# Kernel optimization log

Measured on AMD Instinct MI355X. Metric: run time of the kernel, lower is better.

Reference implementation:

```python
import jax, jax.numpy as jnp
import numpy as np

NIN, NOUT = 256, 64

def setup_inputs() -> dict:
    key = jax.random.key(0)
    k1, k2, k3, k4 = jax.random.split(key, 4)
    B, T = 4, 4096
    y = jax.random.normal(k1, (B, T, NIN), dtype=jnp.float32)
    # torch Linear(nin, nout).weight has shape [nout, nin]; store as [nin, nout]
    s = 1.0 / np.sqrt(NIN)
    Wq = jax.random.uniform(k2, (NIN, NOUT), jnp.float32, -s, s)
    Wk = jax.random.uniform(k3, (NIN, NOUT), jnp.float32, -s, s)
    Wv = jax.random.uniform(k4, (NIN, NOUT), jnp.float32, -s, s)
    return {"y": y, "Wq": Wq, "Wk": Wk, "Wv": Wv}

def reference(y, Wq, Wk, Wv):
    T = y.shape[1]
    que = y @ Wq  # [B,T,NOUT]
    key = y @ Wk
    val = y @ Wv
    att = jnp.einsum('bqd,bkd->bqk', que, key)  # [B,T,T]
    causal = jnp.tril(jnp.ones((T, T), dtype=bool))  # True = keep
    att = jnp.where(causal, att, -jnp.inf)
    att = jax.nn.softmax(att / jnp.sqrt(jnp.float32(NOUT)), axis=-1)
    return jnp.einsum('bqk,bkd->bqd', att, val)
```

## Files before the change

### kernel.cpp

```cpp
#include <hip/hip_runtime.h>
#include <hip/hip_bf16.h>

#define TLEN 4096
#define NINP 256
#define DD   64

#define QSCALE 0.18033688011112042f

typedef __attribute__((ext_vector_type(8))) short bf16x8;
typedef __attribute__((ext_vector_type(4))) short bf16x4;
typedef __attribute__((ext_vector_type(4))) float f32x4;

union U8 { bf16x8 v; uint u[4]; };
union U4 { bf16x4 v; uint u[2]; };

__device__ inline ushort bfu(float x) {
    union { float f; uint u; } a; a.f = x;
    uint r = a.u + 0x7fffu + ((a.u >> 16) & 1u);
    return (ushort)(r >> 16);
}
__device__ inline uint pk2(float lo, float hi) {
    return (uint)bfu(lo) | ((uint)bfu(hi) << 16);
}

__device__ inline bf16x8 ld16(const ushort* p) {
    return *(const bf16x8*)p;
}
__device__ inline bf16x8 ld8x2(const ushort* p) {
    U8 u;
    uint2 a = *(const uint2*)p;
    uint2 b = *(const uint2*)(p + 4);
    u.u[0] = a.x; u.u[1] = a.y; u.u[2] = b.x; u.u[3] = b.y;
    return u.v;
}

__global__ __launch_bounds__(256) void prep_wt(
    const float* __restrict__ Wq, const float* __restrict__ Wk,
    const float* __restrict__ Wv, ushort* __restrict__ WT)
{
    __shared__ ushort lt[256 * 66];
    const int t = threadIdx.x;
    const int m = blockIdx.x;
    const float* W = (m == 0) ? Wq : ((m == 1) ? Wk : Wv);
    const float scale = (m == 0) ? QSCALE : 1.0f;

    #pragma unroll
    for (int j = 0; j < 16; ++j) {
        int i4 = t + 256 * j;
        float4 v = *(const float4*)&W[i4 * 4];
        int k = i4 >> 4, d = (i4 * 4) & 63;
        *(uint*)&lt[k * 66 + d]     = pk2(v.x * scale, v.y * scale);
        *(uint*)&lt[k * 66 + d + 2] = pk2(v.z * scale, v.w * scale);
    }
    __syncthreads();
    #pragma unroll
    for (int j = 0; j < 32; ++j) {
        int o2 = t + 256 * j;
        int d = o2 >> 7, k = (o2 & 127) * 2;
        uint pk = (uint)lt[k * 66 + d] | ((uint)lt[(k + 1) * 66 + d] << 16);
        *(uint*)&WT[m * 16384 + d * 256 + k] = pk;
    }
}

__global__ __launch_bounds__(256, 3) void qkv_kernel(
    const float* __restrict__ y, const ushort* __restrict__ WT,
    ushort* __restrict__ Qh, ushort* __restrict__ Kp, ushort* __restrict__ Vp,
    const int rbn)
{
    __shared__ ushort Wl[64 * 268];
    __shared__ ushort tb[64 * 68];

    const int t = threadIdx.x;
    const int w = t >> 6, lane = t & 63;
    const int quad = lane >> 4, l15 = lane & 15;
    const int mb = blockIdx.x / rbn;
    const int rb = blockIdx.x % rbn;
    const int rowbase = rb * 64;
    const int myrow = rowbase + w * 16 + l15;

    {
        int n = t >> 2, seg = t & 3;
        const ushort* src = WT + mb * 16384 + n * 256 + seg * 64;
        ushort* dst = &Wl[n * 268 + seg * 64];
        #pragma unroll
        for (int j = 0; j < 16; ++j)
            ((uint2*)dst)[j] = ((const uint2*)src)[j];
    }

    bf16x8 afrag[8];
    const float* yrow = y + (size_t)myrow * NINP;
    #pragma unroll
    for (int s = 0; s < 8; ++s) {
        float4 lo = *(const float4*)&yrow[s * 32 + quad * 8];
        float4 hi = *(const float4*)&yrow[s * 32 + quad * 8 + 4];
        U8 u;
        u.u[0] = pk2(lo.x, lo.y);
        u.u[1] = pk2(lo.z, lo.w);
        u.u[2] = pk2(hi.x, hi.y);
        u.u[3] = pk2(hi.z, hi.w);
        afrag[s] = u.v;
    }

    __syncthreads();

    f32x4 acc[4];
    #pragma unroll
    for (int nt = 0; nt < 4; ++nt) acc[nt] = f32x4{0.f, 0.f, 0.f, 0.f};

    #pragma unroll
    for (int s = 0; s < 8; ++s)
        #pragma unroll
        for (int nt = 0; nt < 4; ++nt) {
            bf16x8 bfrag = ld8x2(&Wl[(nt * 16 + l15) * 268 + s * 32 + quad * 8]);
            acc[nt] = __builtin_amdgcn_mfma_f32_16x16x32_bf16(
                afrag[s], bfrag, acc[nt], 0, 0, 0);
        }

    if (mb == 0) {
        #pragma unroll
        for (int nt = 0; nt < 4; ++nt)
            #pragma unroll
            for (int r = 0; r < 4; ++r)
                tb[(w * 16 + quad * 4 + r) * 68 + nt * 16 + l15] = bfu(acc[nt][r]);
        __syncthreads();
        int row = t >> 2, seg = t & 3;
        ushort* gd = Qh + (size_t)(rowbase + row) * DD + seg * 16;
        const ushort* sp = &tb[row * 68 + seg * 16];
        #pragma unroll
        for (int j = 0; j < 4; ++j) ((uint2*)gd)[j] = ((const uint2*)sp)[j];
    } else if (mb == 1) {
        #pragma unroll
        for (int nt = 0; nt < 4; ++nt)
            #pragma unroll
            for (int r = 0; r < 4; ++r)
                tb[(w * 16 + quad * 4 + r) * 68 + nt * 16 + l15] = bfu(acc[nt][r]);
        __syncthreads();
        #pragma unroll
        for (int j = 0; j < 2; ++j) {
            int idx = t + 256 * j;
            int instr = idx >> 6, ln = idx & 63;
            int kt = instr >> 1, s = instr & 1;
            int q2 = ln >> 4, l15b = ln & 15;
            int row = kt * 16 + l15b, dcol = s * 32 + q2 * 8;
            const ushort* sp = &tb[row * 68 + dcol];
            ushort* gd = Kp + (size_t)rb * 4096 + idx * 8;
            ((uint2*)gd)[0] = ((const uint2*)sp)[0];
            ((uint2*)gd)[1] = ((const uint2*)sp)[1];
        }
    } else {
        #pragma unroll
        for (int nt = 0; nt < 4; ++nt) {
            int d = nt * 16 + l15;
            #pragma unroll
            for (int r = 0; r < 4; r += 2) {
                int tt = w * 16 + quad * 4 + r;
                *(uint*)&tb[d * 68 + tt] = pk2(acc[nt][r], acc[nt][r + 1]);
            }
        }
        __syncthreads();
        #pragma unroll
        for (int j = 0; j < 2; ++j) {
            int idx = t + 256 * j;
            int instr = idx >> 6, ln = idx & 63;
            int nt = instr >> 1, m = instr & 1;
            int q2 = ln >> 4, l15b = ln & 15;
            int d = nt * 16 + l15b;
            int k0 = 32 * m + q2 * 4;
            ushort* gd = Vp + (size_t)rb * 4096 + idx * 8;
            ((uint2*)gd)[0] = *(const uint2*)&tb[d * 68 + k0];
            ((uint2*)gd)[1] = *(const uint2*)&tb[d * 68 + k0 + 16];
        }
    }
}

__device__ inline void load_k32(bf16x8 (&kf)[2][2], const ushort* __restrict__ Kw,
                                int ci)
{
    const ushort* base = Kw + (size_t)ci * 2048;
    #pragma unroll
    for (int kt = 0; kt < 2; ++kt)
        #pragma unroll
        for (int s = 0; s < 2; ++s)
            kf[kt][s] = ld16(base + (kt * 2 + s) * 512);
}

__device__ inline void load_v32(U4 (&vt)[4][2], const ushort* __restrict__ Vw,
                                int ci)
{
    const ushort* base = Vw + (size_t)(ci >> 1) * 4096 + (ci & 1) * 512;
    #pragma unroll
    for (int nt = 0; nt < 4; ++nt) {
        U8 uu; uu.v = ld16(base + nt * 1024);
        vt[nt][0].u[0] = uu.u[0]; vt[nt][0].u[1] = uu.u[1];
        vt[nt][1].u[0] = uu.u[2]; vt[nt][1].u[1] = uu.u[3];
    }
}

__global__ __launch_bounds__(512, 4) void attn_kernel(
    const ushort* __restrict__ Qh, const ushort* __restrict__ Kp,
    const ushort* __restrict__ Vp, float* __restrict__ out)
{
    __shared__ float Ob[8][32 * 68];
    __shared__ float lb[8][32];

    const int t = threadIdx.x;
    const int w = t >> 6, lane = t & 63;
    const int quad = lane >> 4, l15 = lane & 15;

    const int x  = blockIdx.x & 7;
    const int b  = x >> 1;
    const int r_ = (int)blockIdx.x >> 3;
    const int h  = r_ >> 5;
    const int j0 = ((r_ & 31) << 1) | (x & 1);
    const int tile = h ? (127 - j0) : j0;

    const int seg = w;
    const int qb  = tile * 32;
    const int nc  = tile + 1;
    const int cps = (nc + 7) >> 3;
    const int clo = seg * cps;
    const int chi = (nc < clo + cps) ? nc : (clo + cps);

    const ushort* Qb = Qh + (size_t)b * TLEN * DD;
    const ushort* Kw = Kp + (size_t)b * 64 * 4096 + lane * 8;
    const ushort* Vw = Vp + (size_t)b * 64 * 4096 + lane * 8;
    float* outb = out + (size_t)b * TLEN * DD;

    f32x4 oT[2][4];
    #pragma unroll
    for (int qt = 0; qt < 2; ++qt)
        #pragma unroll
        for (int nt = 0; nt < 4; ++nt)
            oT[qt][nt] = f32x4{0.f, 0.f, 0.f, 0.f};
    float l_acc[2] = {0.f, 0.f};

    if (clo < chi) {
        bf16x8 qf[2][2];
        #pragma unroll
        for (int qt = 0; qt < 2; ++qt)
            #pragma unroll
            for (int s = 0; s < 2; ++s)
                qf[qt][s] = ld16(Qb + (size_t)(qb + qt * 16 + l15) * DD + s * 32 + quad * 8);

        bf16x8 kf[2][2];
        load_k32(kf, Kw, clo);

        for (int ci = clo; ci < chi; ++ci) {
            const int c0 = ci * 32;

            U4 vt[4][2];
            load_v32(vt, Vw, ci);

            f32x4 st[2][2];
            #pragma unroll
            for (int qt = 0; qt < 2; ++qt)
                #pragma unroll
                for (int kt = 0; kt < 2; ++kt)
                    st[qt][kt] = f32x4{0.f, 0.f, 0.f, 0.f};
            __builtin_amdgcn_s_setprio(1);
            #pragma unroll
            for (int s = 0; s < 2; ++s)
                #pragma unroll
                for (int qt = 0; qt < 2; ++qt)
                    #pragma unroll
                    for (int kt = 0; kt < 2; ++kt)
                        st[qt][kt] = __builtin_amdgcn_mfma_f32_16x16x32_bf16(
                            kf[kt][s], qf[qt][s], st[qt][kt], 0, 0, 0);
            __builtin_amdgcn_s_setprio(0);

            if (ci + 1 < chi) load_k32(kf, Kw, ci + 1);

            U4 pa[2][2];
            if (c0 + 31 <= qb) {
                #pragma unroll
                for (int qt = 0; qt < 2; ++qt)
                    #pragma unroll
                    for (int kt = 0; kt < 2; ++kt) {
                        float p0 = exp2f(st[qt][kt][0]);
                        float p1 = exp2f(st[qt][kt][1]);
                        float p2 = exp2f(st[qt][kt][2]);
                        float p3 = exp2f(st[qt][kt][3]);
                        l_acc[qt] += (p0 + p1) + (p2 + p3);
                        pa[qt][kt].u[0] = pk2(p0, p1);
                        pa[qt][kt].u[1] = pk2(p2, p3);
                    }
            } else {
                #pragma unroll
                for (int qt = 0; qt < 2; ++qt) {
                    const int q = qb + qt * 16 + l15;
                    #pragma unroll
                    for (int kt = 0; kt < 2; ++kt) {
                        const int kb0 = c0 + kt * 16 + quad * 4;
                        float p[4];
                        #pragma unroll
                        for (int r = 0; r < 4; ++r) {
                            float e = exp2f(st[qt][kt][r]);
                            p[r] = (kb0 + r <= q) ? e : 0.f;
                            l_acc[qt] += p[r];
                        }
                        pa[qt][kt].u[0] = pk2(p[0], p[1]);
                        pa[qt][kt].u[1] = pk2(p[2], p[3]);
                    }
                }
            }

            __builtin_amdgcn_s_setprio(1);
            #pragma unroll
            for (int qt = 0; qt < 2; ++qt)
                #pragma unroll
                for (int nt = 0; nt < 4; ++nt)
                    #pragma unroll
                    for (int kt = 0; kt < 2; ++kt)
                        oT[qt][nt] = __builtin_amdgcn_mfma_f32_16x16x16bf16_1k(
                            vt[nt][kt].v, pa[qt][kt].v, oT[qt][nt], 0, 0, 0);
            __builtin_amdgcn_s_setprio(0);
        }

        #pragma unroll
        for (int qt = 0; qt < 2; ++qt) {
            l_acc[qt] += __shfl_xor(l_acc[qt], 16, 64);
            l_acc[qt] += __shfl_xor(l_acc[qt], 32, 64);
        }
    }

    #pragma unroll
    for (int qt = 0; qt < 2; ++qt) {
        #pragma unroll
        for (int nt = 0; nt < 4; ++nt)
            #pragma unroll
            for (int r = 0; r < 4; ++r)
                Ob[w][(qt * 16 + l15) * 68 + nt * 16 + quad * 4 + r] = oT[qt][nt][r];
        if (quad == 0) lb[w][qt * 16 + l15] = l_acc[qt];
    }
    __syncthreads();

    #pragma unroll
    for (int e = 0; e < 4; ++e) {
        int idx = t + 512 * e;
        int q = idx >> 6, d = idx & 63;
        float s = 0.f, ls = 0.f;
        #pragma unroll
        for (int ww = 0; ww < 8; ++ww) {
            s += Ob[ww][q * 68 + d];
            ls += lb[ww][q];
        }
        outb[(size_t)(qb + q) * DD + d] = s * __builtin_amdgcn_rcpf(ls);
    }
}

extern "C" void kernel_launch(void* const* d_in, const int* in_sizes, int n_in,
                              void* d_out, int out_size, void* d_ws, size_t ws_size,
                              hipStream_t stream) {
    const float* y  = (const float*)d_in[0];
    const float* Wq = (const float*)d_in[1];
    const float* Wk = (const float*)d_in[2];
    const float* Wv = (const float*)d_in[3];
    float* outp = (float*)d_out;

    const int rows = in_sizes[0] / NINP;
    const int rbn = rows / 64;

    ushort* WT = (ushort*)d_ws;
    ushort* Qh = WT + 3 * 16384;
    ushort* Kp = Qh + (size_t)rows * DD;
    ushort* Vp = Kp + (size_t)rows * DD;

    prep_wt<<<3, 256, 0, stream>>>(Wq, Wk, Wv, WT);
    qkv_kernel<<<3 * rbn, 256, 0, stream>>>(y, WT, Qh, Kp, Vp, rbn);
    attn_kernel<<<rbn * 2, 512, 0, stream>>>(Qh, Kp, Vp, outp);
}
```

Baseline: 103.3 us.

## Pair causal query tiles per block with 12 waves and hardware bf16 packing

Each attention block now handles two query tiles, a short one and its mirrored long one (tile and 127-tile), processed one after the other. This balances causal work per block and halves the grid to 256 blocks of 768 threads. The key range is split across 12 waves instead of 8, with the segment order reversed for the second tile. Softmax probabilities are packed with the v_cvt_pk_bf16_f32 instruction instead of software rounding. The extra syncthreads and larger shared reduction buffer add overhead, and occupancy drops to 2 blocks per CU.

```diff
diff --git a/kernel.cpp b/kernel.cpp
--- a/kernel.cpp
+++ b/kernel.cpp
@@ -21,6 +21,11 @@
 }
 __device__ inline uint pk2(float lo, float hi) {
     return (uint)bfu(lo) | ((uint)bfu(hi) << 16);
+}
+__device__ inline uint cvtpk(float lo, float hi) {
+    uint r;
+    asm("v_cvt_pk_bf16_f32 %0, %1, %2" : "=v"(r) : "v"(lo), "v"(hi));
+    return r;
 }
 
 __device__ inline bf16x8 ld16(const ushort* p) {
@@ -196,12 +201,12 @@
     }
 }
 
-__global__ __launch_bounds__(512, 4) void attn_kernel(
+__global__ __launch_bounds__(768, 2) void attn_kernel(
     const ushort* __restrict__ Qh, const ushort* __restrict__ Kp,
     const ushort* __restrict__ Vp, float* __restrict__ out)
 {
-    __shared__ float Ob[8][32 * 68];
-    __shared__ float lb[8][32];
+    __shared__ float Ob[12][32 * 68];
+    __shared__ float lb[12][32];
 
     const int t = threadIdx.x;
     const int w = t >> 6, lane = t & 63;
@@ -209,142 +214,145 @@
 
     const int x  = blockIdx.x & 7;
     const int b  = x >> 1;
-    const int r_ = (int)blockIdx.x >> 3;
-    const int h  = r_ >> 5;
-    const int j0 = ((r_ & 31) << 1) | (x & 1);
-    const int tile = h ? (127 - j0) : j0;
-
-    const int seg = w;
-    const int qb  = tile * 32;
-    const int nc  = tile + 1;
-    const int cps = (nc + 7) >> 3;
-    const int clo = seg * cps;
-    const int chi = (nc < clo + cps) ? nc : (clo + cps);
+    const int pr = (((int)blockIdx.x >> 3) << 1) | (x & 1);
 
     const ushort* Qb = Qh + (size_t)b * TLEN * DD;
     const ushort* Kw = Kp + (size_t)b * 64 * 4096 + lane * 8;
     const ushort* Vw = Vp + (size_t)b * 64 * 4096 + lane * 8;
     float* outb = out + (size_t)b * TLEN * DD;
 
-    f32x4 oT[2][4];
-    #pragma unroll
-    for (int qt = 0; qt < 2; ++qt)
-        #pragma unroll
-        for (int nt = 0; nt < 4; ++nt)
-            oT[qt][nt] = f32x4{0.f, 0.f, 0.f, 0.f};
-    float l_acc[2] = {0.f, 0.f};
-
-    if (clo < chi) {
-        bf16x8 qf[2][2];
+    for (int half = 0; half < 2; ++half) {
+        const int tile = half ? (127 - pr) : pr;
+        const int seg  = half ? (11 - w) : w;
+        const int qb   = tile * 32;
+        const int nc   = tile + 1;
+        const int cps  = (nc + 11) / 12;
+        const int clo  = seg * cps;
+        const int chi  = (nc < clo + cps) ? nc : (clo + cps);
+
+        f32x4 oT[2][4];
         #pragma unroll
         for (int qt = 0; qt < 2; ++qt)
             #pragma unroll
-            for (int s = 0; s < 2; ++s)
-                qf[qt][s] = ld16(Qb + (size_t)(qb + qt * 16 + l15) * DD + s * 32 + quad * 8);
-
-        bf16x8 kf[2][2];
-        load_k32(kf, Kw, clo);
-
-        for (int ci = clo; ci < chi; ++ci) {
-            const int c0 = ci * 32;
-
-            U4 vt[4][2];
-            load_v32(vt, Vw, ci);
-
-            f32x4 st[2][2];
+            for (int nt = 0; nt < 4; ++nt)
+                oT[qt][nt] = f32x4{0.f, 0.f, 0.f, 0.f};
+        float l_acc[2] = {0.f, 0.f};
+
+        if (clo < chi) {
+            bf16x8 qf[2][2];
             #pragma unroll
             for (int qt = 0; qt < 2; ++qt)
                 #pragma unroll
-                for (int kt = 0; kt < 2; ++kt)
-                    st[qt][kt] = f32x4{0.f, 0.f, 0.f, 0.f};
-            __builtin_amdgcn_s_setprio(1);
-            #pragma unroll
-            for (int s = 0; s < 2; ++s)
+                for (int s = 0; s < 2; ++s)
+                    qf[qt][s] = ld16(Qb + (size_t)(qb + qt * 16 + l15) * DD + s * 32 + quad * 8);
+
+            bf16x8 kf[2][2];
+            load_k32(kf, Kw, clo);
+
+            for (int ci = clo; ci < chi; ++ci) {
+                const int c0 = ci * 32;
+
+                U4 vt[4][2];
+                load_v32(vt, Vw, ci);
+
+                f32x4 st[2][2];
                 #pragma unroll
                 for (int qt = 0; qt < 2; ++qt)
                     #pragma unroll
                     for (int kt = 0; kt < 2; ++kt)
-                        st[qt][kt] = __builtin_amdgcn_mfma_f32_16x16x32_bf16(
-                            kf[kt][s], qf[qt][s], st[qt][kt], 0, 0, 0);
-            __builtin_amdgcn_s_setprio(0);
-
-            if (ci + 1 < chi) load_k32(kf, Kw, ci + 1);
-
-            U4 pa[2][2];
-            if (c0 + 31 <= qb) {
-                #pragma unroll
-                for (int qt = 0; qt < 2; ++qt)
-                    #pragma unroll
-                    for (int kt = 0; kt < 2; ++kt) {
-                        float p0 = exp2f(st[qt][kt][0]);
-                        float p1 = exp2f(st[qt][kt][1]);
-                        float p2 = exp2f(st[qt][kt][2]);
-                        float p3 = exp2f(st[qt][kt][3]);
-                        l_acc[qt] += (p0 + p1) + (p2 + p3);
-                        pa[qt][kt].u[0] = pk2(p0, p1);
-                        pa[qt][kt].u[1] = pk2(p2, p3);
-                    }
-            } else {
-                #pragma unroll
-                for (int qt = 0; qt < 2; ++qt) {
-                    const int q = qb + qt * 16 + l15;
-                    #pragma unroll
-                    for (int kt = 0; kt < 2; ++kt) {
-                        const int kb0 = c0 + kt * 16 + quad * 4;
-                        float p[4];
+                        st[qt][kt] = f32x4{0.f, 0.f, 0.f, 0.f};
+                __builtin_amdgcn_s_setprio(1);
+                #pragma unroll
+                for (int s = 0; s < 2; ++s)
+                    #pragma unroll
+                    for (int qt = 0; qt < 2; ++qt)
                         #pragma unroll
-                        for (int r = 0; r < 4; ++r) {
-                            float e = exp2f(st[qt][kt][r]);
-                            p[r] = (kb0 + r <= q) ? e : 0.f;
-                            l_acc[qt] += p[r];
+                        for (int kt = 0; kt < 2; ++kt)
+                            st[qt][kt] = __builtin_amdgcn_mfma_f32_16x16x32_bf16(
+                                kf[kt][s], qf[qt][s], st[qt][kt], 0, 0, 0);
+                __builtin_amdgcn_s_setprio(0);
+
+                if (ci + 1 < chi) load_k32(kf, Kw, ci + 1);
+
+                U4 pa[2][2];
+                if (c0 + 31 <= qb) {
+                    #pragma unroll
+                    for (int qt = 0; qt < 2; ++qt)
+                        #pragma unroll
+                        for (int kt = 0; kt < 2; ++kt) {
+                            float p0 = exp2f(st[qt][kt][0]);
+                            float p1 = exp2f(st[qt][kt][1]);
+                            float p2 = exp2f(st[qt][kt][2]);
+                            float p3 = exp2f(st[qt][kt][3]);
+                            l_acc[qt] += (p0 + p1) + (p2 + p3);
+                            pa[qt][kt].u[0] = cvtpk(p0, p1);
+                            pa[qt][kt].u[1] = cvtpk(p2, p3);
                         }
-                        pa[qt][kt].u[0] = pk2(p[0], p[1]);
-                        pa[qt][kt].u[1] = pk2(p[2], p[3]);
+                } else {
+                    #pragma unroll
+                    for (int qt = 0; qt < 2; ++qt) {
+                        const int q = qb + qt * 16 + l15;
+                        #pragma unroll
+                        for (int kt = 0; kt < 2; ++kt) {
+                            const int kb0 = c0 + kt * 16 + quad * 4;
+                            float p[4];
+                            #pragma unroll
+                            for (int r = 0; r < 4; ++r) {
+                                float e = exp2f(st[qt][kt][r]);
+                                p[r] = (kb0 + r <= q) ? e : 0.f;
+                                l_acc[qt] += p[r];
+                            }
+                            pa[qt][kt].u[0] = cvtpk(p[0], p[1]);
+                            pa[qt][kt].u[1] = cvtpk(p[2], p[3]);
+                        }
                     }
                 }
+
+                __builtin_amdgcn_s_setprio(1);
+                #pragma unroll
+                for (int qt = 0; qt < 2; ++qt)
+                    #pragma unroll
+                    for (int nt = 0; nt < 4; ++nt)
+                        #pragma unroll
+                        for (int kt = 0; kt < 2; ++kt)
+                            oT[qt][nt] = __builtin_amdgcn_mfma_f32_16x16x16bf16_1k(
+                                vt[nt][kt].v, pa[qt][kt].v, oT[qt][nt], 0, 0, 0);
+                __builtin_amdgcn_s_setprio(0);
             }
 
-            __builtin_amdgcn_s_setprio(1);
-            #pragma unroll
-            for (int qt = 0; qt < 2; ++qt)
-                #pragma unroll
-                for (int nt = 0; nt < 4; ++nt)
-                    #pragma unroll
-                    for (int kt = 0; kt < 2; ++kt)
-                        oT[qt][nt] = __builtin_amdgcn_mfma_f32_16x16x16bf16_1k(
-                            vt[nt][kt].v, pa[qt][kt].v, oT[qt][nt], 0, 0, 0);
-            __builtin_amdgcn_s_setprio(0);
+            #pragma unroll
+            for (int qt = 0; qt < 2; ++qt) {
+                l_acc[qt] += __shfl_xor(l_acc[qt], 16, 64);
+                l_acc[qt] += __shfl_xor(l_acc[qt], 32, 64);
+            }
         }
 
         #pragma unroll
         for (int qt = 0; qt < 2; ++qt) {
-            l_acc[qt] += __shfl_xor(l_acc[qt], 16, 64);
-            l_acc[qt] += __shfl_xor(l_acc[qt], 32, 64);
-        }
-    }
-
-    #pragma unroll
-    for (int qt = 0; qt < 2; ++qt) {
-        #pragma unroll
-        for (int nt = 0; nt < 4; ++nt)
-            #pragma unroll
-            for (int r = 0; r < 4; ++r)
-                Ob[w][(qt * 16 + l15) * 68 + nt * 16 + quad * 4 + r] = oT[qt][nt][r];
-        if (quad == 0) lb[w][qt * 16 + l15] = l_acc[qt];
-    }
-    __syncthreads();
-
-    #pragma unroll
-    for (int e = 0; e < 4; ++e) {
-        int idx = t + 512 * e;
-        int q = idx >> 6, d = idx & 63;
-        float s = 0.f, ls = 0.f;
-        #pragma unroll
-        for (int ww = 0; ww < 8; ++ww) {
-            s += Ob[ww][q * 68 + d];
-            ls += lb[ww][q];
-        }
-        outb[(size_t)(qb + q) * DD + d] = s * __builtin_amdgcn_rcpf(ls);
+            #pragma unroll
+            for (int nt = 0; nt < 4; ++nt)
+                #pragma unroll
+                for (int r = 0; r < 4; ++r)
+                    Ob[w][(qt * 16 + l15) * 68 + nt * 16 + quad * 4 + r] = oT[qt][nt][r];
+            if (quad == 0) lb[w][qt * 16 + l15] = l_acc[qt];
+        }
+        __syncthreads();
+
+        #pragma unroll
+        for (int e = 0; e < 3; ++e) {
+            int idx = t + 768 * e;
+            if (idx < 2048) {
+                int q = idx >> 6, d = idx & 63;
+                float s = 0.f, ls = 0.f;
+                #pragma unroll
+                for (int ww = 0; ww < 12; ++ww) {
+                    s += Ob[ww][q * 68 + d];
+                    ls += lb[ww][q];
+                }
+                outb[(size_t)(qb + q) * DD + d] = s * __builtin_amdgcn_rcpf(ls);
+            }
+        }
+        __syncthreads();
     }
 }
 
@@ -358,6 +366,7 @@
     float* outp = (float*)d_out;
 
     const int rows = in_sizes[0] / NINP;
+    const int nb = rows / TLEN;
     const int rbn = rows / 64;
 
     ushort* WT = (ushort*)d_ws;
@@ -367,5 +376,5 @@
 
     prep_wt<<<3, 256, 0, stream>>>(Wq, Wk, Wv, WT);
     qkv_kernel<<<3 * rbn, 256, 0, stream>>>(y, WT, Qh, Kp, Vp, rbn);
-    attn_kernel<<<rbn * 2, 512, 0, stream>>>(Qh, Kp, Vp, outp);
-}
+    attn_kernel<<<nb * 64, 768, 0, stream>>>(Qh, Kp, Vp, outp);
+}
```

Result: no change. 101.4 us (-1.8%).
